# Kernel tuning notes

Hardware: AMD Instinct MI355X
Metric: run time of the kernel (lower is better)

The kernel has to match this reference:

```python
import jax, jax.numpy as jnp
import numpy as np

N_NODES = 100000
N_EDGES = 3200000
IN_DIM, HID_DIM, OUT_DIM = 128, 64, 3


def gcn_conv(x, edge_index, W, b):
    """PyG GCNConv: add self-loops, symmetric deg^{-1/2} normalization,
    linear transform then scatter-sum aggregation, plus bias."""
    n = x.shape[0]
    loop = jnp.arange(n, dtype=edge_index.dtype)
    src = jnp.concatenate([edge_index[0], loop])  # [E+N]
    dst = jnp.concatenate([edge_index[1], loop])
    deg = jax.ops.segment_sum(jnp.ones_like(dst, dtype=x.dtype), dst, num_segments=n)
    dinv = jax.lax.rsqrt(jnp.maximum(deg, 1.0))  # deg >= 1 due to self-loops
    norm = dinv[src] * dinv[dst]                 # [E+N]
    h = x @ W                                    # [N, F_out]
    msgs = h[src] * norm[:, None]                # gather + scale
    out = jax.ops.segment_sum(msgs, dst, num_segments=n)
    return out + b


def setup_inputs() -> dict:
    key = jax.random.key(0)
    k1, k2, k3, k4 = jax.random.split(key, 4)
    x = jax.random.normal(k1, (N_NODES, IN_DIM), dtype=jnp.float32)
    edge_index = jax.random.randint(k2, (2, N_EDGES), 0, N_NODES, dtype=jnp.int64)
    W1 = jax.random.normal(k3, (IN_DIM, HID_DIM), dtype=jnp.float32) * (1.0 / np.sqrt(IN_DIM))
    b1 = jnp.zeros((HID_DIM,), dtype=jnp.float32)
    W2 = jax.random.normal(k4, (HID_DIM, OUT_DIM), dtype=jnp.float32) * (1.0 / np.sqrt(HID_DIM))
    b2 = jnp.zeros((OUT_DIM,), dtype=jnp.float32)
    return {"x": x, "edge_index": edge_index, "W1": W1, "b1": b1, "W2": W2, "b2": b2}


def reference(x, edge_index, W1, b1, W2, b2):
    h = gcn_conv(x, edge_index, W1, b1)
    h = jax.nn.relu(h)
    out = gcn_conv(h, edge_index, W2, b2)
    return out
```

## Files before the change

kernel.cpp:

```cpp
#include <hip/hip_runtime.h>
#include <hip/hip_fp16.h>
#include <cstdint>
#include <cstddef>

#define DIM_IN 128
#define DIM_HID 64
#define MS_TILE 4096
#define OVF_CAP 32768
#define BSH 8
#define BINSZ 256
#define MAXNB 512
#define CAPL 10240

typedef int v2i __attribute__((ext_vector_type(2)));

__global__ void k_detect(const int* __restrict__ e, int* __restrict__ flag) {
    if (blockIdx.x == 0 && threadIdx.x == 0) {
        int o = 0;
        for (int j = 1; j < 128; j += 2) o |= e[j];
        flag[0] = (o == 0) ? 2 : 1;
    }
}

__global__ __launch_bounds__(256) void k_msplit2(const int* __restrict__ eidx,
                                                 const int* __restrict__ flag,
                                                 int* __restrict__ binCursor,
                                                 unsigned int* __restrict__ binned,
                                                 int* __restrict__ ovfCnt,
                                                 v2i* __restrict__ ovf,
                                                 int E, int NB, int cap) {
    __shared__ int hist[MAXNB], base[MAXNB], scanb[MAXNB], s4[128];
    __shared__ v2i buf[MS_TILE];
    int t = threadIdx.x;
    int st = flag[0];
    int ntiles = (E + MS_TILE - 1) / MS_TILE;

    for (int tile = blockIdx.x; tile < ntiles; tile += gridDim.x) {
        int e0 = tile * MS_TILE;
        int cntE = min(MS_TILE, E - e0);

        unsigned int words[16];
        int bins[16];
#pragma unroll
        for (int j = 0; j < 16; j++) {
            int e = e0 + t + 256 * j;
            if (e < E) {
                int s, d;
                if (st == 2) {
                    v2i a = __builtin_nontemporal_load((const v2i*)eidx + e);
                    v2i b = __builtin_nontemporal_load((const v2i*)eidx + E + e);
                    s = a.x; d = b.x;
                } else {
                    s = __builtin_nontemporal_load(&eidx[e]);
                    d = __builtin_nontemporal_load(&eidx[E + e]);
                }
                words[j] = ((unsigned int)s << BSH) | (unsigned int)(d & (BINSZ - 1));
                bins[j] = d >> BSH;
            } else {
                bins[j] = -1;
            }
        }

        hist[t] = 0; hist[t + 256] = 0;
        __syncthreads();
#pragma unroll
        for (int j = 0; j < 16; j++)
            if (bins[j] >= 0) atomicAdd(&hist[bins[j]], 1);
        __syncthreads();
        if (t < 128)
            s4[t] = hist[4 * t] + hist[4 * t + 1] + hist[4 * t + 2] + hist[4 * t + 3];
        __syncthreads();
        if (t == 0) {
            int run = 0;
            for (int b = 0; b < 128; b++) { int v = s4[b]; s4[b] = run; run += v; }
        }
        __syncthreads();
        if (t < 128) {
            int r = s4[t];
#pragma unroll
            for (int j = 0; j < 4; j++) { scanb[4 * t + j] = r; r += hist[4 * t + j]; }
        }
        __syncthreads();
        for (int b = t; b < NB; b += 256)
            if (hist[b] > 0) base[b] = atomicAdd(&binCursor[b], hist[b]);
        __syncthreads();
        hist[t] = 0; hist[t + 256] = 0;
        __syncthreads();
#pragma unroll
        for (int j = 0; j < 16; j++) {
            if (bins[j] >= 0) {
                int r = atomicAdd(&hist[bins[j]], 1);
                buf[scanb[bins[j]] + r] = (v2i){(int)words[j], bins[j]};
            }
        }
        __syncthreads();
        for (int j = t; j < cntE; j += 256) {
            v2i p = buf[j];
            int b = p.y;
            int local = base[b] + (j - scanb[b]);
            if (local < cap) {
                binned[(size_t)b * cap + local] = (unsigned int)p.x;
            } else {
                int o = atomicAdd(ovfCnt, 1);
                if (o < OVF_CAP)
                    ovf[o] = (v2i){(int)((unsigned int)p.x >> BSH),
                                   (b << BSH) | (p.x & (BINSZ - 1))};
            }
        }
        __syncthreads();
    }
}

__global__ __launch_bounds__(512) void k_binscan(const int* __restrict__ binCursor,
                                                 int* __restrict__ binBase,
                                                 int NB, int cap) {
    __shared__ int sh[512];
    int t = threadIdx.x;
    int v = (t < NB) ? min(binCursor[t], cap) : 0;
    sh[t] = v;
    __syncthreads();
    for (int d = 1; d < 512; d <<= 1) {
        int add = (t >= d) ? sh[t - d] : 0;
        __syncthreads();
        sh[t] += add;
        __syncthreads();
    }
    if (t < NB) binBase[t] = sh[t] - v;
}

__global__ __launch_bounds__(256) void k_fillA(const unsigned int* __restrict__ binned,
                                               const int* __restrict__ binCursor,
                                               const int* __restrict__ binBase,
                                               int* __restrict__ offsets,
                                               int* __restrict__ cursor,
                                               float* __restrict__ dinv,
                                               int* __restrict__ csr,
                                               int cap, int N) {
    __shared__ int hist[BINSZ], scanS[BINSZ], curL[BINSZ];
    __shared__ unsigned int stage[CAPL];
    int b = blockIdx.x;
    int t = threadIdx.x;
    int g0 = b << BSH;
    int g = g0 + t;
    int n = min(binCursor[b], cap);
    const unsigned int* p = binned + (size_t)b * cap;

    hist[t] = 0;
    __syncthreads();
    for (int i = t; i < n; i += 256)
        atomicAdd(&hist[__builtin_nontemporal_load(p + i) & (BINSZ - 1)], 1);
    __syncthreads();
    int h = hist[t];
    scanS[t] = h;
    __syncthreads();
    for (int d = 1; d < 256; d <<= 1) {
        int add = (t >= d) ? scanS[t - d] : 0;
        __syncthreads();
        scanS[t] += add;
        __syncthreads();
    }
    int excl = scanS[t] - h;
    int gbase = binBase[b];
    if (g < N) {
        offsets[g] = gbase + excl;
        dinv[g] = rsqrtf((float)(h + 1));
    }
    if (t == 255) offsets[min(g0 + BINSZ, N)] = gbase + scanS[255];

    curL[t] = excl;
    __syncthreads();
    int nl = min(n, CAPL);
    for (int i = t; i < nl; i += 256) {
        unsigned int w = __builtin_nontemporal_load(p + i);
        int pos = atomicAdd(&curL[w & (BINSZ - 1)], 1);
        if (pos < CAPL) stage[pos] = w >> BSH;
    }
    __syncthreads();
    if (g < N) cursor[g] = gbase + curL[t];
    for (int i = t; i < nl; i += 256)
        csr[gbase + i] = (int)stage[i];
    __syncthreads();
    for (int i = CAPL + t; i < n; i += 256) {
        unsigned int w = p[i];
        int pos = atomicAdd(&cursor[g0 + (int)(w & (BINSZ - 1))], 1);
        csr[pos] = (int)(w >> BSH);
    }
}

__global__ void k_ovf(const int* __restrict__ ovfCnt, const v2i* __restrict__ ovf,
                      int* __restrict__ cursor, int* __restrict__ csr) {
    int n = min(*ovfCnt, OVF_CAP);
    for (int i = threadIdx.x; i < n; i += 256) {
        v2i e = ovf[i];
        int pos = atomicAdd(&cursor[e.y], 1);
        csr[pos] = e.x;
    }
}

__global__ __launch_bounds__(256) void k_gemm1t(const float* __restrict__ x,
                                                const float* __restrict__ W,
                                                const float* __restrict__ dinv,
                                                __half2* __restrict__ h1, int N) {
    __shared__ float xsT[DIM_IN * 64];
    __shared__ float Ws[DIM_IN * DIM_HID];
    int t = threadIdx.x;
    int row0 = blockIdx.x * 64;

#pragma unroll
    for (int i = 0; i < 8; i++)
        ((float4*)Ws)[t + 256 * i] = ((const float4*)W)[t + 256 * i];

#pragma unroll
    for (int i = 0; i < 8; i++) {
        int idx = t * 8 + i;
        int r = idx >> 5;
        int kc = idx & 31;
        int row = row0 + r;
        float4 v = (row < N) ? ((const float4*)(x + (size_t)row * DIM_IN))[kc]
                             : make_float4(0.f, 0.f, 0.f, 0.f);
        xsT[(4 * kc + 0) * 64 + r] = v.x;
        xsT[(4 * kc + 1) * 64 + r] = v.y;
        xsT[(4 * kc + 2) * 64 + r] = v.z;
        xsT[(4 * kc + 3) * 64 + r] = v.w;
    }
    __syncthreads();

    int c = t & 15;
    int r = t >> 4;
    float acc[4][4] = {};

#pragma unroll 4
    for (int k = 0; k < DIM_IN; k++) {
        float4 xa = *(const float4*)&xsT[k * 64 + 4 * r];
        float4 wb = *(const float4*)&Ws[k * DIM_HID + 4 * c];
#pragma unroll
        for (int i = 0; i < 4; i++) {
            float xi = (i == 0) ? xa.x : (i == 1) ? xa.y : (i == 2) ? xa.z : xa.w;
            acc[i][0] = fmaf(xi, wb.x, acc[i][0]);
            acc[i][1] = fmaf(xi, wb.y, acc[i][1]);
            acc[i][2] = fmaf(xi, wb.z, acc[i][2]);
            acc[i][3] = fmaf(xi, wb.w, acc[i][3]);
        }
    }

#pragma unroll
    for (int i = 0; i < 4; i++) {
        int row = row0 + 4 * r + i;
        if (row < N) {
            float d = dinv[row];
            h1[(size_t)row * 32 + 2 * c] = __floats2half2_rn(acc[i][0] * d, acc[i][1] * d);
            h1[(size_t)row * 32 + 2 * c + 1] = __floats2half2_rn(acc[i][2] * d, acc[i][3] * d);
        }
    }
}

__global__ __launch_bounds__(256) void k_agg1(const __half2* __restrict__ h1,
                                              const int* __restrict__ csr,
                                              const int* __restrict__ offsets,
                                              const float* __restrict__ dinv,
                                              const float* __restrict__ b1,
                                              const float* __restrict__ W2,
                                              float4* __restrict__ h2, int N) {
    int t = threadIdx.x;
    int hl = t & 31;
    int node = blockIdx.x * 8 + (t >> 5);
    if (node >= N) return;

    float di = dinv[node];
    int beg = offsets[node], end = offsets[node + 1];
    __half2 a0 = h1[(size_t)node * 32 + hl];
    __half2 a1 = __floats2half2_rn(0.f, 0.f);

    for (int base = beg; base < end; base += 32) {
        int rem = min(32, end - base);
        int sidx = (hl < rem) ? csr[base + hl] : 0;
        if (rem == 32) {
#pragma unroll 8
            for (int j = 0; j < 32; j += 4) {
                int s0 = __shfl(sidx, j, 32);
                int s1 = __shfl(sidx, j + 1, 32);
                int s2 = __shfl(sidx, j + 2, 32);
                int s3 = __shfl(sidx, j + 3, 32);
                a0 = __hadd2(a0, h1[(size_t)s0 * 32 + hl]);
                a1 = __hadd2(a1, h1[(size_t)s1 * 32 + hl]);
                a0 = __hadd2(a0, h1[(size_t)s2 * 32 + hl]);
                a1 = __hadd2(a1, h1[(size_t)s3 * 32 + hl]);
            }
        } else {
            int j = 0;
            for (; j + 1 < rem; j += 2) {
                int s0 = __shfl(sidx, j, 32);
                int s1 = __shfl(sidx, j + 1, 32);
                a0 = __hadd2(a0, h1[(size_t)s0 * 32 + hl]);
                a1 = __hadd2(a1, h1[(size_t)s1 * 32 + hl]);
            }
            if (j < rem) {
                int s0 = __shfl(sidx, j, 32);
                a0 = __hadd2(a0, h1[(size_t)s0 * 32 + hl]);
            }
        }
    }

    float2 f0 = __half22float2(a0);
    float2 f1 = __half22float2(a1);
    float accx = f0.x + f1.x, accy = f0.y + f1.y;

    float2 bb = ((const float2*)b1)[hl];
    float gx = fmaxf(fmaf(accx, di, bb.x), 0.f);
    float gy = fmaxf(fmaf(accy, di, bb.y), 0.f);

    const float* w0 = W2 + (2 * hl) * 3;
    const float* w1 = W2 + (2 * hl + 1) * 3;
    float v0 = gx * w0[0] + gy * w1[0];
    float v1 = gx * w0[1] + gy * w1[1];
    float v2 = gx * w0[2] + gy * w1[2];
#pragma unroll
    for (int off = 16; off > 0; off >>= 1) {
        v0 += __shfl_xor(v0, off, 64);
        v1 += __shfl_xor(v1, off, 64);
        v2 += __shfl_xor(v2, off, 64);
    }
    if (hl == 0) h2[node] = make_float4(v0 * di, v1 * di, v2 * di, 0.f);
}

__global__ __launch_bounds__(256) void k_agg2(const float4* __restrict__ h2,
                                              const int* __restrict__ csr,
                                              const int* __restrict__ offsets,
                                              const float* __restrict__ dinv,
                                              const float* __restrict__ b2,
                                              float* __restrict__ out, int N) {
    int t = threadIdx.x;
    int lane = t & 63;
    int node = blockIdx.x * 4 + (t >> 6);
    if (node >= N) return;

    float di = dinv[node];
    int beg = offsets[node], end = offsets[node + 1];
    float a0 = 0.f, a1 = 0.f, a2 = 0.f;
    for (int e = beg + lane; e < end; e += 64) {
        float4 h = h2[csr[e]];
        a0 += h.x;
        a1 += h.y;
        a2 += h.z;
    }
#pragma unroll
    for (int off = 32; off > 0; off >>= 1) {
        a0 += __shfl_xor(a0, off, 64);
        a1 += __shfl_xor(a1, off, 64);
        a2 += __shfl_xor(a2, off, 64);
    }
    if (lane == 0) {
        float4 hs = h2[node];
        out[(size_t)node * 3 + 0] = fmaf(a0 + hs.x, di, b2[0]);
        out[(size_t)node * 3 + 1] = fmaf(a1 + hs.y, di, b2[1]);
        out[(size_t)node * 3 + 2] = fmaf(a2 + hs.z, di, b2[2]);
    }
}

extern "C" void kernel_launch(void* const* d_in, const int* in_sizes, int n_in,
                              void* d_out, int out_size, void* d_ws, size_t ws_size,
                              hipStream_t stream) {
    const float* x = (const float*)d_in[0];
    const int* eidx = (const int*)d_in[1];
    const float* W1 = (const float*)d_in[2];
    const float* b1 = (const float*)d_in[3];
    const float* W2 = (const float*)d_in[4];
    const float* b2 = (const float*)d_in[5];
    float* out = (float*)d_out;

    const int N = in_sizes[0] / DIM_IN;
    const int E = in_sizes[1] / 2;
    const int NB = (N + BINSZ - 1) >> BSH;

    char* w = (char*)d_ws;
    size_t off = 0;
    auto carve = [&](size_t bytes) -> char* {
        char* p = w + off;
        off += (bytes + 255) & ~(size_t)255;
        return p;
    };
    int* flag = (int*)carve(16);
    int* offsets = (int*)carve((size_t)(N + 1) * 4);
    int* cursor = (int*)carve((size_t)N * 4);
    float* dinv = (float*)carve((size_t)N * 4);
    int* csr = (int*)carve((size_t)E * 4);
    int* binCursor = (int*)carve(MAXNB * 4);
    int* ovfCnt = (int*)carve(16);
    v2i* ovf = (v2i*)carve((size_t)OVF_CAP * 8);
    int* binBase = (int*)carve(MAXNB * 4);
    float4* h2 = (float4*)carve((size_t)N * 16);

    size_t h1_bytes = (size_t)N * DIM_HID * 2;
    int capDes = E / NB + E / NB / 16 + 128;
    size_t binned_des = (size_t)NB * capDes * 4;
    size_t uni_avail = (ws_size > off + 256) ? (ws_size - off - 256) : h1_bytes;
    size_t uni_bytes = binned_des > h1_bytes ? binned_des : h1_bytes;
    if (uni_bytes > uni_avail) uni_bytes = uni_avail > h1_bytes ? uni_avail : h1_bytes;
    char* uni = carve(uni_bytes);
    unsigned int* binned = (unsigned int*)uni;
    __half2* h1 = (__half2*)uni;
    int cap = (int)(uni_bytes / ((size_t)NB * 4));
    if (cap > capDes) cap = capDes;
    if (cap > CAPL) cap = CAPL;

    (void)hipMemsetAsync(binCursor, 0, MAXNB * 4 + 256, stream);
    k_detect<<<1, 64, 0, stream>>>(eidx, flag);

    int ntiles = (E + MS_TILE - 1) / MS_TILE;
    k_msplit2<<<ntiles, 256, 0, stream>>>(eidx, flag, binCursor, binned,
                                          ovfCnt, ovf, E, NB, cap);
    k_binscan<<<1, 512, 0, stream>>>(binCursor, binBase, NB, cap);
    k_fillA<<<NB, 256, 0, stream>>>(binned, binCursor, binBase, offsets, cursor,
                                    dinv, csr, cap, N);
    k_ovf<<<1, 256, 0, stream>>>(ovfCnt, ovf, cursor, csr);

    k_gemm1t<<<(N + 63) / 64, 256, 0, stream>>>(x, W1, dinv, h1, N);
    k_agg1<<<(N + 7) / 8, 256, 0, stream>>>(h1, csr, offsets, dinv, b1, W2, h2, N);
    k_agg2<<<(N + 3) / 4, 256, 0, stream>>>(h2, csr, offsets, dinv, b2, out, N);
}
```

Before: 197.7 us.

## Simplify edge binning pass, fold dtype detection, narrow agg2 to 8 lanes per node

```diff
diff --git a/kernel.cpp b/kernel.cpp
--- a/kernel.cpp
+++ b/kernel.cpp
@@ -5,7 +5,7 @@
 
 #define DIM_IN 128
 #define DIM_HID 64
-#define MS_TILE 4096
+#define MS_TILE 8192
 #define OVF_CAP 32768
 #define BSH 8
 #define BINSZ 256
@@ -14,71 +14,33 @@
 
 typedef int v2i __attribute__((ext_vector_type(2)));
 
-__global__ void k_detect(const int* __restrict__ e, int* __restrict__ flag) {
-    if (blockIdx.x == 0 && threadIdx.x == 0) {
-        int o = 0;
-        for (int j = 1; j < 128; j += 2) o |= e[j];
-        flag[0] = (o == 0) ? 2 : 1;
-    }
-}
-
-__global__ __launch_bounds__(256) void k_msplit2(const int* __restrict__ eidx,
-                                                 const int* __restrict__ flag,
+__global__ __launch_bounds__(256) void k_msplit3(const int* __restrict__ eidx,
                                                  int* __restrict__ binCursor,
                                                  unsigned int* __restrict__ binned,
                                                  int* __restrict__ ovfCnt,
                                                  v2i* __restrict__ ovf,
                                                  int E, int NB, int cap) {
-    __shared__ int hist[MAXNB], base[MAXNB], scanb[MAXNB], s4[128];
-    __shared__ v2i buf[MS_TILE];
-    int t = threadIdx.x;
-    int st = flag[0];
+    __shared__ int hist[MAXNB], base[MAXNB];
+    __shared__ int stF;
+    int t = threadIdx.x;
+    if (t == 0) {
+        int o = 0;
+        for (int j = 1; j < 128; j += 2) o |= eidx[j];
+        stF = (o == 0) ? 2 : 1;
+    }
+    __syncthreads();
+    int st = stF;
     int ntiles = (E + MS_TILE - 1) / MS_TILE;
 
     for (int tile = blockIdx.x; tile < ntiles; tile += gridDim.x) {
         int e0 = tile * MS_TILE;
-        int cntE = min(MS_TILE, E - e0);
-
-        unsigned int words[16];
-        int bins[16];
-#pragma unroll
-        for (int j = 0; j < 16; j++) {
-            int e = e0 + t + 256 * j;
-            if (e < E) {
-                int s, d;
-                if (st == 2) {
-                    v2i a = __builtin_nontemporal_load((const v2i*)eidx + e);
-                    v2i b = __builtin_nontemporal_load((const v2i*)eidx + E + e);
-                    s = a.x; d = b.x;
-                } else {
-                    s = __builtin_nontemporal_load(&eidx[e]);
-                    d = __builtin_nontemporal_load(&eidx[E + e]);
-                }
-                words[j] = ((unsigned int)s << BSH) | (unsigned int)(d & (BINSZ - 1));
-                bins[j] = d >> BSH;
-            } else {
-                bins[j] = -1;
-            }
-        }
+        int e1 = min(e0 + MS_TILE, E);
 
         hist[t] = 0; hist[t + 256] = 0;
         __syncthreads();
-#pragma unroll
-        for (int j = 0; j < 16; j++)
-            if (bins[j] >= 0) atomicAdd(&hist[bins[j]], 1);
-        __syncthreads();
-        if (t < 128)
-            s4[t] = hist[4 * t] + hist[4 * t + 1] + hist[4 * t + 2] + hist[4 * t + 3];
-        __syncthreads();
-        if (t == 0) {
-            int run = 0;
-            for (int b = 0; b < 128; b++) { int v = s4[b]; s4[b] = run; run += v; }
-        }
-        __syncthreads();
-        if (t < 128) {
-            int r = s4[t];
-#pragma unroll
-            for (int j = 0; j < 4; j++) { scanb[4 * t + j] = r; r += hist[4 * t + j]; }
+        for (int e = e0 + t; e < e1; e += 256) {
+            int d = eidx[(size_t)(E + e) * st];
+            atomicAdd(&hist[d >> BSH], 1);
         }
         __syncthreads();
         for (int b = t; b < NB; b += 256)
@@ -86,25 +48,18 @@
         __syncthreads();
         hist[t] = 0; hist[t + 256] = 0;
         __syncthreads();
-#pragma unroll
-        for (int j = 0; j < 16; j++) {
-            if (bins[j] >= 0) {
-                int r = atomicAdd(&hist[bins[j]], 1);
-                buf[scanb[bins[j]] + r] = (v2i){(int)words[j], bins[j]};
-            }
-        }
-        __syncthreads();
-        for (int j = t; j < cntE; j += 256) {
-            v2i p = buf[j];
-            int b = p.y;
-            int local = base[b] + (j - scanb[b]);
+        for (int e = e0 + t; e < e1; e += 256) {
+            int s = eidx[(size_t)e * st];
+            int d = eidx[(size_t)(E + e) * st];
+            int b = d >> BSH;
+            int r = atomicAdd(&hist[b], 1);
+            int local = base[b] + r;
             if (local < cap) {
-                binned[(size_t)b * cap + local] = (unsigned int)p.x;
+                binned[(size_t)b * cap + local] =
+                    ((unsigned int)s << BSH) | (unsigned int)(d & (BINSZ - 1));
             } else {
                 int o = atomicAdd(ovfCnt, 1);
-                if (o < OVF_CAP)
-                    ovf[o] = (v2i){(int)((unsigned int)p.x >> BSH),
-                                   (b << BSH) | (p.x & (BINSZ - 1))};
+                if (o < OVF_CAP) ovf[o] = (v2i){s, d};
             }
         }
         __syncthreads();
@@ -148,7 +103,7 @@
     hist[t] = 0;
     __syncthreads();
     for (int i = t; i < n; i += 256)
-        atomicAdd(&hist[__builtin_nontemporal_load(p + i) & (BINSZ - 1)], 1);
+        atomicAdd(&hist[p[i] & (BINSZ - 1)], 1);
     __syncthreads();
     int h = hist[t];
     scanS[t] = h;
@@ -171,7 +126,7 @@
     __syncthreads();
     int nl = min(n, CAPL);
     for (int i = t; i < nl; i += 256) {
-        unsigned int w = __builtin_nontemporal_load(p + i);
+        unsigned int w = p[i];
         int pos = atomicAdd(&curL[w & (BINSZ - 1)], 1);
         if (pos < CAPL) stage[pos] = w >> BSH;
     }
@@ -330,26 +285,26 @@
                                               const float* __restrict__ b2,
                                               float* __restrict__ out, int N) {
     int t = threadIdx.x;
-    int lane = t & 63;
-    int node = blockIdx.x * 4 + (t >> 6);
+    int l = t & 7;
+    int node = blockIdx.x * 32 + (t >> 3);
     if (node >= N) return;
 
     float di = dinv[node];
     int beg = offsets[node], end = offsets[node + 1];
     float a0 = 0.f, a1 = 0.f, a2 = 0.f;
-    for (int e = beg + lane; e < end; e += 64) {
+    for (int e = beg + l; e < end; e += 8) {
         float4 h = h2[csr[e]];
         a0 += h.x;
         a1 += h.y;
         a2 += h.z;
     }
 #pragma unroll
-    for (int off = 32; off > 0; off >>= 1) {
-        a0 += __shfl_xor(a0, off, 64);
-        a1 += __shfl_xor(a1, off, 64);
-        a2 += __shfl_xor(a2, off, 64);
-    }
-    if (lane == 0) {
+    for (int off = 4; off > 0; off >>= 1) {
+        a0 += __shfl_xor(a0, off, 8);
+        a1 += __shfl_xor(a1, off, 8);
+        a2 += __shfl_xor(a2, off, 8);
+    }
+    if (l == 0) {
         float4 hs = h2[node];
         out[(size_t)node * 3 + 0] = fmaf(a0 + hs.x, di, b2[0]);
         out[(size_t)node * 3 + 1] = fmaf(a1 + hs.y, di, b2[1]);
@@ -379,7 +334,6 @@
         off += (bytes + 255) & ~(size_t)255;
         return p;
     };
-    int* flag = (int*)carve(16);
     int* offsets = (int*)carve((size_t)(N + 1) * 4);
     int* cursor = (int*)carve((size_t)N * 4);
     float* dinv = (float*)carve((size_t)N * 4);
@@ -404,11 +358,10 @@
     if (cap > CAPL) cap = CAPL;
 
     (void)hipMemsetAsync(binCursor, 0, MAXNB * 4 + 256, stream);
-    k_detect<<<1, 64, 0, stream>>>(eidx, flag);
 
     int ntiles = (E + MS_TILE - 1) / MS_TILE;
-    k_msplit2<<<ntiles, 256, 0, stream>>>(eidx, flag, binCursor, binned,
-                                          ovfCnt, ovf, E, NB, cap);
+    k_msplit3<<<ntiles, 256, 0, stream>>>(eidx, binCursor, binned, ovfCnt, ovf,
+                                          E, NB, cap);
     k_binscan<<<1, 512, 0, stream>>>(binCursor, binBase, NB, cap);
     k_fillA<<<NB, 256, 0, stream>>>(binned, binCursor, binBase, offsets, cursor,
                                     dinv, csr, cap, N);
@@ -416,5 +369,5 @@
 
     k_gemm1t<<<(N + 63) / 64, 256, 0, stream>>>(x, W1, dinv, h1, N);
     k_agg1<<<(N + 7) / 8, 256, 0, stream>>>(h1, csr, offsets, dinv, b1, W2, h2, N);
-    k_agg2<<<(N + 3) / 4, 256, 0, stream>>>(h2, csr, offsets, dinv, b2, out, N);
-}
+    k_agg2<<<(N + 31) / 32, 256, 0, stream>>>(h2, csr, offsets, dinv, b2, out, N);
+}
```

New measurement: 193.1 us. 1.02x faster.
